# Kernel tuning notes

Measured on AMD Instinct MI355X. Metric: run time of the kernel, lower is better.

Reference implementation:

```python
import jax, jax.numpy as jnp
import numpy as np

B, N, IN_DIM, HID, OUT_DIM = 8, 1024, 768, 128, 768
H1, H2, MHA_HEADS, C = 8, 1, 4, 32
ALPHA = 0.2
NEG = -9e15
LN_EPS = 1e-5


def _gat_layer(x, W, a1, a2, adj_mask):
    # x: [B,N,Fin], W: [H,Fin,Fout], a1/a2: [H,Fout], adj_mask: [B,N,N] bool
    h = jnp.einsum('bni,hio->bhno', x, W)                      # [B,H,N,F]
    s1 = jnp.einsum('bhno,ho->bhn', h, a1)                     # score for source node i
    s2 = jnp.einsum('bhno,ho->bhn', h, a2)                     # score for target node j
    e = jax.nn.leaky_relu(s1[:, :, :, None] + s2[:, :, None, :], negative_slope=ALPHA)
    e = jnp.where(adj_mask[:, None, :, :], e, NEG)
    attn = jax.nn.softmax(e, axis=-1)                          # [B,H,N,N]
    hp = jnp.einsum('bhnm,bhmo->bhno', attn, h)                # [B,H,N,F]
    b, nh, n, f = hp.shape
    return hp.transpose(0, 2, 1, 3).reshape(b, n, nh * f)      # concat heads -> [B,N,H*F]


def _mha(q, k, v, wq, bq, wk, bk, wv, bv, wo, bo, n_heads):
    # torch-style MultiheadAttention (eval, no dropout). q:[B,Lq,E] k,v:[B,Lk,E]
    b, lq, e = q.shape
    lk = k.shape[1]
    hd = e // n_heads
    Q = (q @ wq + bq).reshape(b, lq, n_heads, hd).transpose(0, 2, 1, 3)
    K = (k @ wk + bk).reshape(b, lk, n_heads, hd).transpose(0, 2, 1, 3)
    V = (v @ wv + bv).reshape(b, lk, n_heads, hd).transpose(0, 2, 1, 3)
    scores = jnp.einsum('bhqd,bhkd->bhqk', Q, K) / jnp.sqrt(jnp.float32(hd))
    attn = jax.nn.softmax(scores, axis=-1)
    out = jnp.einsum('bhqk,bhkd->bhqd', attn, V)
    out = out.transpose(0, 2, 1, 3).reshape(b, lq, e)
    return out @ wo + bo


def _layernorm(x, g, b):
    mu = jnp.mean(x, axis=-1, keepdims=True)
    var = jnp.var(x, axis=-1, keepdims=True)
    return (x - mu) * jax.lax.rsqrt(var + LN_EPS) * g + b


def setup_inputs() -> dict:
    key = jax.random.key(0)
    ks = jax.random.split(key, 24)
    s = lambda fan_in: 1.0 / np.sqrt(fan_in)
    inp = {
        'node_features': jax.random.normal(ks[0], (B, N, IN_DIM), jnp.float32),
        'adjacency': jax.random.randint(ks[1], (B, N, N), 0, 2, jnp.int32),
        'context_indices': jax.random.randint(ks[2], (B, C), 0, N, jnp.int32),
        # GAT layer 1: 8 heads, in=768 -> out=128 each
        'W1': jax.random.normal(ks[3], (H1, IN_DIM, HID), jnp.float32) * s(IN_DIM),
        'a1_1': jax.random.normal(ks[4], (H1, HID), jnp.float32) * s(2 * HID),
        'a2_1': jax.random.normal(ks[5], (H1, HID), jnp.float32) * s(2 * HID),
        # GAT layer 2: 1 head, in=1024 -> out=128
        'W2': jax.random.normal(ks[6], (H2, HID * H1, HID), jnp.float32) * s(HID * H1),
        'a1_2': jax.random.normal(ks[7], (H2, HID), jnp.float32) * s(2 * HID),
        'a2_2': jax.random.normal(ks[8], (H2, HID), jnp.float32) * s(2 * HID),
        # query MultiheadAttention (embed_dim=128, 4 heads)
        'wq': jax.random.normal(ks[9], (HID, HID), jnp.float32) * s(HID),
        'bq': jnp.zeros((HID,), jnp.float32),
        'wk': jax.random.normal(ks[10], (HID, HID), jnp.float32) * s(HID),
        'bk': jnp.zeros((HID,), jnp.float32),
        'wv': jax.random.normal(ks[11], (HID, HID), jnp.float32) * s(HID),
        'bv': jnp.zeros((HID,), jnp.float32),
        'wo': jax.random.normal(ks[12], (HID, HID), jnp.float32) * s(HID),
        'bo': jnp.zeros((HID,), jnp.float32),
        # projection MLP
        'p1_w': jax.random.normal(ks[13], (HID, HID), jnp.float32) * s(HID),
        'p1_b': jnp.zeros((HID,), jnp.float32),
        'ln_g': jnp.ones((HID,), jnp.float32),
        'ln_b': jnp.zeros((HID,), jnp.float32),
        'p2_w': jax.random.normal(ks[14], (HID, OUT_DIM), jnp.float32) * s(HID),
        'p2_b': jnp.zeros((OUT_DIM,), jnp.float32),
    }
    return inp


def reference(node_features, adjacency, context_indices,
              W1, a1_1, a2_1, W2, a1_2, a2_2,
              wq, bq, wk, bk, wv, bv, wo, bo,
              p1_w, p1_b, ln_g, ln_b, p2_w, p2_b):
    adj_mask = adjacency > 0
    h = jax.nn.elu(_gat_layer(node_features, W1, a1_1, a2_1, adj_mask))  # [B,N,1024]
    h = jax.nn.elu(_gat_layer(h, W2, a1_2, a2_2, adj_mask))              # [B,N,128]
    q = h[:, 0:1, :]                                                      # [B,1,E]
    ctx = jnp.take_along_axis(h, context_indices[:, :, None], axis=1)     # [B,C,E]
    pooled = _mha(q, ctx, ctx, wq, bq, wk, bk, wv, bv, wo, bo, MHA_HEADS)[:, 0, :]
    z = jax.nn.relu(_layernorm(pooled @ p1_w + p1_b, ln_g, ln_b))
    return z @ p2_w + p2_b                                                # [B,OUT_DIM]
```

## Files before the change

### kernel.cpp

```cpp
#include <hip/hip_runtime.h>
#include <hip/hip_bf16.h>

#define ALPHA 0.2f
#define LOG2E 1.4426950408889634f

using short8  = __attribute__((ext_vector_type(8))) short;
using short4v = __attribute__((ext_vector_type(4))) short;
using f32x4   = __attribute__((ext_vector_type(4))) float;
using int4v   = __attribute__((ext_vector_type(4))) int;

static __device__ __forceinline__ float b2f(short s) {
    union { float f; unsigned u; } v; v.u = ((unsigned)(unsigned short)s) << 16; return v.f;
}
static __device__ __forceinline__ short f2bf(float f) {
    __hip_bfloat16 h = __float2bfloat16(f);
    return *reinterpret_cast<short*>(&h);
}
static __device__ __forceinline__ float fexp2(float x) {
    return __builtin_amdgcn_exp2f(x);
}
static __device__ __forceinline__ void gload_lds16(const void* g, void* l) {
    __builtin_amdgcn_global_load_lds(
        (const __attribute__((address_space(1))) unsigned*)g,
        (__attribute__((address_space(3))) unsigned*)l, 16, 0, 0);
}

__global__ __launch_bounds__(256) void k_prep(
        const int* __restrict__ adj, unsigned* __restrict__ adjb,
        const float* __restrict__ x, short* __restrict__ xb,
        const float* __restrict__ W1, short* __restrict__ W1T,
        const float* __restrict__ W2, short* __restrict__ W2T) {
    int bid = blockIdx.x, t = threadIdx.x;
    if (bid < 32768) {
        int idx = bid * 256 + t;
        int lane = t & 63;
        unsigned long long m = __ballot(adj[idx] > 0);
        if ((lane & 31) == 0) adjb[idx >> 5] = (unsigned)(m >> (lane & 32));
    } else if (bid < 38912) {
        int idx = (bid - 32768) * 256 + t;
        f32x4 v = ((const f32x4*)x)[idx];
        short4v o;
        o[0] = f2bf(v[0]); o[1] = f2bf(v[1]); o[2] = f2bf(v[2]); o[3] = f2bf(v[3]);
        ((short4v*)xb)[idx] = o;
    } else if (bid < 41984) {
        int idx = (bid - 38912) * 256 + t;
        int n = idx / 768, k = idx - n * 768;
        int h = n >> 7, o = n & 127;
        W1T[idx] = f2bf(W1[(h * 768 + k) * 128 + o]);
    } else {
        int idx = (bid - 41984) * 256 + t;
        int n = idx >> 10, k = idx & 1023;
        W2T[idx] = f2bf(W2[k * 128 + n]);
    }
}

__global__ __launch_bounds__(256) void k_gemm_bt(
        const short* __restrict__ A, const short* __restrict__ Bt,
        short* __restrict__ Ct, int K, int Ncols,
        const float* __restrict__ a1, const float* __restrict__ a2,
        float* __restrict__ s1, float* __restrict__ s2) {
    int tid = threadIdx.x, wave = tid >> 6, lane = tid & 63;
    int lr = lane & 15, lg = lane >> 4;
    int flat = blockIdx.y * gridDim.x + blockIdx.x;
    int chunkw = (gridDim.x * gridDim.y) >> 3;
    int swz = (flat & 7) * chunkw + (flat >> 3);
    int bx = swz % gridDim.x, by = swz / gridDim.x;
    int m0 = bx * 128, n0 = by * 128;
    int wm = (wave >> 1) * 64, wn = (wave & 1) * 64;
    __shared__ short lsA[2][128 * 64], lsB[2][128 * 64];
    __shared__ float sred1[2][128], sred2[2][128];
    f32x4 acc[4][4];
#pragma unroll
    for (int i = 0; i < 4; i++)
#pragma unroll
        for (int j = 0; j < 4; j++) acc[i][j] = (f32x4){0.f, 0.f, 0.f, 0.f};

    auto stage = [&](int bufsel, int k0) {
#pragma unroll
        for (int s = 0; s < 4; s++) {
            int chunk = s * 256 + tid;
            int r = chunk >> 3, c = chunk & 7;
            int csrc = c ^ (r & 7);
            gload_lds16(A + (size_t)(m0 + r) * K + k0 + csrc * 8, &lsA[bufsel][chunk * 8]);
            gload_lds16(Bt + (size_t)(n0 + r) * K + k0 + csrc * 8, &lsB[bufsel][chunk * 8]);
        }
    };
    auto compute = [&](const short* la, const short* lb) {
#pragma unroll
        for (int kk = 0; kk < 2; kk++) {
            short8 a[4], bb[4];
#pragma unroll
            for (int f = 0; f < 4; f++) {
                int ra = wm + f * 16 + lr, rb = wn + f * 16 + lr;
                a[f]  = *(const short8*)(la + ra * 64 + (((kk * 4 + lg) ^ (ra & 7)) * 8));
                bb[f] = *(const short8*)(lb + rb * 64 + (((kk * 4 + lg) ^ (rb & 7)) * 8));
            }
#pragma unroll
            for (int fm = 0; fm < 4; fm++)
#pragma unroll
                for (int fn = 0; fn < 4; fn++)
                    acc[fm][fn] = __builtin_amdgcn_mfma_f32_16x16x32_bf16(a[fm], bb[fn], acc[fm][fn], 0, 0, 0);
        }
    };
    stage(0, 0);
    __syncthreads();
    for (int k2 = 0; k2 < K; k2 += 128) {
        stage(1, k2 + 64);
        compute(lsA[0], lsB[0]);
        __syncthreads();
        if (k2 + 128 < K) stage(0, k2 + 128);
        compute(lsA[1], lsB[1]);
        __syncthreads();
    }
#pragma unroll
    for (int fm = 0; fm < 4; fm++) {
        int mb = m0 + wm + fm * 16 + lg * 4;
        size_t obase = ((size_t)(mb >> 10) * Ncols) * 1024 + (mb & 1023);
#pragma unroll
        for (int fn = 0; fn < 4; fn++) {
            int n = n0 + wn + fn * 16 + lr;
            short4v st;
            st[0] = f2bf(acc[fm][fn][0]); st[1] = f2bf(acc[fm][fn][1]);
            st[2] = f2bf(acc[fm][fn][2]); st[3] = f2bf(acc[fm][fn][3]);
            *(short4v*)(Ct + obase + (size_t)n * 1024) = st;
        }
    }
    if (a1 != nullptr) {
        int h = by;
        float av1[4], av2[4];
#pragma unroll
        for (int fn = 0; fn < 4; fn++) {
            int o = wn + fn * 16 + lr;
            av1[fn] = a1[h * 128 + o];
            av2[fn] = a2[h * 128 + o];
        }
        int wcol = wave & 1;
#pragma unroll
        for (int fm = 0; fm < 4; fm++)
#pragma unroll
            for (int r = 0; r < 4; r++) {
                float v1 = acc[fm][0][r] * av1[0] + acc[fm][1][r] * av1[1]
                         + acc[fm][2][r] * av1[2] + acc[fm][3][r] * av1[3];
                float v2 = acc[fm][0][r] * av2[0] + acc[fm][1][r] * av2[1]
                         + acc[fm][2][r] * av2[2] + acc[fm][3][r] * av2[3];
#pragma unroll
                for (int off = 1; off < 16; off <<= 1) {
                    v1 += __shfl_xor(v1, off);
                    v2 += __shfl_xor(v2, off);
                }
                if (lr == 0) {
                    int il = wm + fm * 16 + lg * 4 + r;
                    sred1[wcol][il] = v1;
                    sred2[wcol][il] = v2;
                }
            }
        __syncthreads();
        if (tid < 128) {
            int b = m0 >> 10;
            int irow = (b * 8 + h) * 1024 + (m0 & 1023) + tid;
            s1[irow] = (sred1[0][tid] + sred1[1][tid]) * LOG2E;
            s2[irow] = (sred2[0][tid] + sred2[1][tid]) * LOG2E;
        }
    }
}

__global__ __launch_bounds__(256) void k_gemm64(
        const short* __restrict__ A, const short* __restrict__ Bt,
        short* __restrict__ Ct, int K, int Ncols) {
    int tid = threadIdx.x, wave = tid >> 6, lane = tid & 63;
    int lr = lane & 15, lg = lane >> 4;
    int flat = blockIdx.y * gridDim.x + blockIdx.x;
    int chunkw = (gridDim.x * gridDim.y) >> 3;
    int swz = (flat & 7) * chunkw + (flat >> 3);
    int bx = swz % gridDim.x, by = swz / gridDim.x;
    int m0 = bx * 64, n0 = by * 64;
    int wm = (wave >> 1) * 32, wn = (wave & 1) * 32;
    __shared__ short lsA[2][64 * 32], lsB[2][64 * 32];
    f32x4 acc[2][2];
#pragma unroll
    for (int i = 0; i < 2; i++)
#pragma unroll
        for (int j = 0; j < 2; j++) acc[i][j] = (f32x4){0.f, 0.f, 0.f, 0.f};

    auto stage = [&](int bufsel, int k0) {
        int r = tid >> 2, c = tid & 3;
        int csrc = c ^ (r & 3);
        int base = (wave * 64) * 8;
        gload_lds16(A + (size_t)(m0 + r) * K + k0 + csrc * 8, &lsA[bufsel][base]);
        gload_lds16(Bt + (size_t)(n0 + r) * K + k0 + csrc * 8, &lsB[bufsel][base]);
    };
    stage(0, 0);
    __syncthreads();
    int buf = 0;
    for (int k0 = 0; k0 < K; k0 += 32) {
        if (k0 + 32 < K) stage(buf ^ 1, k0 + 32);
        short8 a[2], bb[2];
#pragma unroll
        for (int f = 0; f < 2; f++) {
            int ra = wm + f * 16 + lr, rb = wn + f * 16 + lr;
            a[f]  = *(const short8*)(&lsA[buf][ra * 32 + ((lg ^ (ra & 3)) * 8)]);
            bb[f] = *(const short8*)(&lsB[buf][rb * 32 + ((lg ^ (rb & 3)) * 8)]);
        }
#pragma unroll
        for (int fm = 0; fm < 2; fm++)
#pragma unroll
            for (int fn = 0; fn < 2; fn++)
                acc[fm][fn] = __builtin_amdgcn_mfma_f32_16x16x32_bf16(a[fm], bb[fn], acc[fm][fn], 0, 0, 0);
        __syncthreads();
        buf ^= 1;
    }
#pragma unroll
    for (int fm = 0; fm < 2; fm++) {
        int mb = m0 + wm + fm * 16 + lg * 4;
        size_t obase = ((size_t)(mb >> 10) * Ncols) * 1024 + (mb & 1023);
#pragma unroll
        for (int fn = 0; fn < 2; fn++) {
            int n = n0 + wn + fn * 16 + lr;
            short4v st;
            st[0] = f2bf(acc[fm][fn][0]); st[1] = f2bf(acc[fm][fn][1]);
            st[2] = f2bf(acc[fm][fn][2]); st[3] = f2bf(acc[fm][fn][3]);
            *(short4v*)(Ct + obase + (size_t)n * 1024) = st;
        }
    }
}

__global__ __launch_bounds__(256) void k_s12(
        const short* __restrict__ ht, const float* __restrict__ a1,
        const float* __restrict__ a2, float* __restrict__ s1,
        float* __restrict__ s2, int nh) {
    int bh = blockIdx.x;
    int h = bh % nh;
    int i4 = threadIdx.x * 4;
    const short* base = ht + (size_t)bh * 131072 + i4;
    f32x4 acc1 = {0.f, 0.f, 0.f, 0.f}, acc2 = {0.f, 0.f, 0.f, 0.f};
#pragma unroll 8
    for (int o = 0; o < 128; o++) {
        short4v v = *(const short4v*)(base + ((size_t)o << 10));
        float w1 = a1[h * 128 + o], w2 = a2[h * 128 + o];
#pragma unroll
        for (int r = 0; r < 4; r++) {
            float f = b2f(v[r]);
            acc1[r] += f * w1;
            acc2[r] += f * w2;
        }
    }
#pragma unroll
    for (int r = 0; r < 4; r++) { acc1[r] *= LOG2E; acc2[r] *= LOG2E; }
    *(f32x4*)(s1 + bh * 1024 + i4) = acc1;
    *(f32x4*)(s2 + bh * 1024 + i4) = acc2;
}

__global__ __launch_bounds__(512) void k_attn1(
        const short* __restrict__ ht, const unsigned* __restrict__ adjb,
        const float* __restrict__ s1, const float* __restrict__ s2,
        short* __restrict__ out) {
    int flat = blockIdx.y * 8 + blockIdx.x;
    int swz = (flat & 7) * 64 + (flat >> 3);
    int bh = swz >> 3, bxi = swz & 7;
    int b = bh >> 3, h = bh & 7;
    int tid = threadIdx.x, wave = tid >> 6, lane = tid & 63;
    int lr = lane & 15, lg = lane >> 4;
    int ic = bxi * 128 + wave * 16 + lr;
    int row = bh * 1024 + ic;
    float s1i = s1[row];
    const unsigned long long* abrow =
        (const unsigned long long*)(adjb + ((size_t)(b << 10) + ic) * 32);
    const float* s2r = s2 + bh * 1024;
    const short* hbase = ht + (size_t)bh * 131072;

    __shared__ short lsh[2][16384];
    f32x4 acc[8];
#pragma unroll
    for (int f = 0; f < 8; f++) acc[f] = (f32x4){0.f, 0.f, 0.f, 0.f};
    f32x4 accs = (f32x4){0.f, 0.f, 0.f, 0.f};
    short8 ones8;
#pragma unroll
    for (int e = 0; e < 8; e++) ones8[e] = (short)0x3F80;

    auto stage = [&](int bufsel, int j0) {
#pragma unroll
        for (int s = 0; s < 4; s++) {
            int chunk = s * 512 + tid;
            int r = chunk >> 4, c = chunk & 15;
            int csrc = c ^ (r & 15);
            gload_lds16(hbase + (size_t)r * 1024 + j0 + csrc * 8,
                        &lsh[bufsel][chunk * 8]);
        }
    };
    auto compute = [&](const short* ls, int j0) {
        unsigned long long aw0 = abrow[j0 >> 6], aw1 = abrow[(j0 >> 6) + 1];
#pragma unroll
        for (int kk = 0; kk < 4; kk++) {
            int jb = j0 + kk * 32 + lg * 8;
            f32x4 t0 = *(const f32x4*)(s2r + jb);
            f32x4 t1 = *(const f32x4*)(s2r + jb + 4);
            unsigned long long aw = (kk < 2) ? aw0 : aw1;
            unsigned bits = (unsigned)(aw >> ((kk & 1) * 32 + lg * 8)) & 0xFFu;
            float pv[8];
#pragma unroll
            for (int e = 0; e < 8; e++) {
                float sv = e < 4 ? t0[e] : t1[e & 3];
                float ee = s1i + sv;
                ee = fmaxf(ee, ALPHA * ee);
                float p = fexp2(ee);
                pv[e] = ((bits >> e) & 1) ? p : 0.f;
            }
            int4v pw;
#pragma unroll
            for (int w = 0; w < 4; w++) {
                int d;
                asm("v_cvt_pk_bf16_f32 %0, %1, %2"
                    : "=v"(d) : "v"(pv[2 * w]), "v"(pv[2 * w + 1]));
                pw[w] = d;
            }
            short8 pb = __builtin_bit_cast(short8, pw);
            accs = __builtin_amdgcn_mfma_f32_16x16x32_bf16(ones8, pb, accs, 0, 0, 0);
#pragma unroll
            for (int fm = 0; fm < 8; fm++) {
                int r = fm * 16 + lr;
                int ck = (kk * 4 + lg) ^ (r & 15);
                short8 af = *(const short8*)(ls + r * 128 + ck * 8);
                acc[fm] = __builtin_amdgcn_mfma_f32_16x16x32_bf16(af, pb, acc[fm], 0, 0, 0);
            }
        }
    };

    stage(0, 0);
    __syncthreads();
    for (int t2 = 0; t2 < 1024; t2 += 256) {
        stage(1, t2 + 128);
        compute(lsh[0], t2);
        __syncthreads();
        if (t2 + 256 < 1024) stage(0, t2 + 256);
        compute(lsh[1], t2 + 128);
        __syncthreads();
    }
    float rdi = 1.f / accs[0];
    size_t orow = ((size_t)(b << 10) + ic) * 1024 + h * 128;
#pragma unroll
    for (int fm = 0; fm < 8; fm++) {
        int ob = (fm << 4) + lg * 4;
        short4v st;
#pragma unroll
        for (int r = 0; r < 4; r++) {
            float x = acc[fm][r] * rdi;
            x = x > 0.f ? x : expm1f(x);
            st[r] = f2bf(x);
        }
        *(short4v*)(out + orow + ob) = st;
    }
}

__global__ __launch_bounds__(256) void k_attn2g(
        const short* __restrict__ h2t, const unsigned* __restrict__ adjb,
        const float* __restrict__ s1, const float* __restrict__ s2,
        const int* __restrict__ cidx, float* __restrict__ ghat) {
    int tile = blockIdx.x;
    int b = blockIdx.y;
    int tid = threadIdx.x, wave = tid >> 6, lane = tid & 63;
    int lr = lane & 15, lg = lane >> 4;

    __shared__ int nodes[16];
    __shared__ float sps[4][16];
    __shared__ float sacc[4][16][129];

    if (tid < 16) {
        int pos = tile * 16 + tid;
        int nd = 0;
        if (pos >= 1 && pos <= 32) nd = cidx[b * 32 + pos - 1];
        nodes[tid] = nd;
    }
    __syncthreads();

    const float* s2r = s2 + b * 1024;
    int nd = nodes[lr];
    float s1i = s1[b * 1024 + nd];
    const unsigned long long* abrow =
        (const unsigned long long*)(adjb + ((size_t)(b << 10) + nd) * 32);
    const short* hb = h2t + (size_t)b * 131072;
    f32x4 acc[8];
#pragma unroll
    for (int f = 0; f < 8; f++) acc[f] = (f32x4){0.f, 0.f, 0.f, 0.f};
    float psum = 0.f;

    for (int j0 = wave * 256; j0 < wave * 256 + 256; j0 += 32) {
        int jb = j0 + lg * 8;
        f32x4 t0 = *(const f32x4*)(s2r + jb);
        f32x4 t1 = *(const f32x4*)(s2r + jb + 4);
        unsigned bits = (unsigned)(abrow[j0 >> 6] >> ((j0 & 32) + lg * 8)) & 0xFFu;
        short8 pb;
#pragma unroll
        for (int e = 0; e < 8; e++) {
            float sv = e < 4 ? t0[e] : t1[e & 3];
            float ee = s1i + sv;
            ee = fmaxf(ee, ALPHA * ee);
            float p = fexp2(ee);
            p = ((bits >> e) & 1) ? p : 0.f;
            psum += p;
            pb[e] = f2bf(p);
        }
#pragma unroll
        for (int fm = 0; fm < 8; fm++) {
            short8 af = *(const short8*)(hb + (size_t)(fm * 16 + lr) * 1024 + jb);
            acc[fm] = __builtin_amdgcn_mfma_f32_16x16x32_bf16(af, pb, acc[fm], 0, 0, 0);
        }
    }
    psum += __shfl_xor(psum, 16);
    psum += __shfl_xor(psum, 32);
    if (lg == 0) sps[wave][lr] = psum;
#pragma unroll
    for (int fm = 0; fm < 8; fm++)
#pragma unroll
        for (int r = 0; r < 4; r++)
            sacc[wave][lr][fm * 16 + lg * 4 + r] = acc[fm][r];
    __syncthreads();
    for (int e = tid; e < 2048; e += 256) {
        int li = e >> 7, o = e & 127;
        float sum = sps[0][li] + sps[1][li] + sps[2][li] + sps[3][li];
        float v = (sacc[0][li][o] + sacc[1][li][o] + sacc[2][li][o] + sacc[3][li][o]) / sum;
        v = v > 0.f ? v : expm1f(v);
        ghat[((size_t)b * 48 + tile * 16 + li) * 128 + o] = v;
    }
}

__global__ __launch_bounds__(256) void k_qkv(
        const float* __restrict__ ghat,
        const float* __restrict__ wk, const float* __restrict__ bk,
        const float* __restrict__ wvp, const float* __restrict__ bv,
        float* __restrict__ Kp, float* __restrict__ Vp) {
    int b = blockIdx.y, rg = blockIdx.x & 7, o0 = (blockIdx.x >> 3) * 64;
    int t = threadIdx.x, wvi = t >> 6, ln = t & 63;
    __shared__ float sx[4][128];
    __shared__ float sWk[128 * 64], sWv[128 * 64];

    if (wvi < 2) {
        int cb = wvi * 64;
        gload_lds16(ghat + ((size_t)b * 48 + 1 + rg * 4) * 128 + (size_t)(cb + ln) * 4,
                    (float*)sx + cb * 4);
    }
#pragma unroll
    for (int s = 0; s < 8; s++) {
        int cb = s * 256 + wvi * 64;
        int q = cb + ln, rw = q >> 4, c4 = q & 15;
        gload_lds16(wk  + (size_t)rw * 128 + o0 + c4 * 4, &sWk[cb * 4]);
        gload_lds16(wvp + (size_t)rw * 128 + o0 + c4 * 4, &sWv[cb * 4]);
    }
    __syncthreads();
    int o = o0 + ln;
    float ka = bk[o], va = bv[o];
#pragma unroll 32
    for (int c = 0; c < 128; c++) {
        float x = sx[wvi][c];
        ka += x * sWk[c * 64 + ln];
        va += x * sWv[c * 64 + ln];
    }
    int r = rg * 4 + wvi;
    Kp[((size_t)b * 32 + r) * 128 + o] = ka;
    Vp[((size_t)b * 32 + r) * 128 + o] = va;
}

__global__ __launch_bounds__(256) void k_tail(
        const float* __restrict__ ghat, const float* __restrict__ Kp,
        const float* __restrict__ Vp,
        const float* __restrict__ wq, const float* __restrict__ bq,
        const float* __restrict__ wo, const float* __restrict__ bo,
        const float* __restrict__ p1w, const float* __restrict__ p1b,
        const float* __restrict__ lng, const float* __restrict__ lnb,
        float* __restrict__ tvec) {
    int b = blockIdx.x, t = threadIdx.x;
    int wvi = t >> 6, ln = t & 63;
    __shared__ float sq[128], sQ[128], sK[32][128], sV[32][128];
    __shared__ float sP[4][33], sO[128], sT[128], sZ[128];
    __shared__ float sred[2];
    __shared__ float sW[128 * 128];

#pragma unroll
    for (int s = 0; s < 4; s++) {
        int cb = s * 256 + wvi * 64;
        gload_lds16(Kp + (size_t)b * 4096 + (size_t)(cb + ln) * 4, (float*)sK + cb * 4);
        gload_lds16(Vp + (size_t)b * 4096 + (size_t)(cb + ln) * 4, (float*)sV + cb * 4);
    }
#pragma unroll
    for (int s = 0; s < 16; s++) {
        int cb = s * 256 + wvi * 64;
        gload_lds16(wq + (size_t)(cb + ln) * 4, &sW[cb * 4]);
    }
    if (t < 128) sq[t] = ghat[(size_t)b * 48 * 128 + t];
    __syncthreads();
    if (t < 128) {
        float a0 = 0.f, a1 = 0.f, a2 = 0.f, a3 = 0.f;
#pragma unroll
        for (int c = 0; c < 128; c += 4) {
            a0 += sq[c]     * sW[c * 128 + t];
            a1 += sq[c + 1] * sW[(c + 1) * 128 + t];
            a2 += sq[c + 2] * sW[(c + 2) * 128 + t];
            a3 += sq[c + 3] * sW[(c + 3) * 128 + t];
        }
        sQ[t] = bq[t] + ((a0 + a1) + (a2 + a3));
    }
    __syncthreads();
#pragma unroll
    for (int s = 0; s < 16; s++) {
        int cb = s * 256 + wvi * 64;
        gload_lds16(wo + (size_t)(cb + ln) * 4, &sW[cb * 4]);
    }
    if (t < 128) {
        int hh = t >> 5, jj = t & 31;
        float s = 0.f;
#pragma unroll
        for (int d = 0; d < 32; d++) s += sQ[hh * 32 + d] * sK[jj][hh * 32 + d];
        s *= 0.17677669529663687f;
        float m = s;
#pragma unroll
        for (int off = 16; off > 0; off >>= 1) m = fmaxf(m, __shfl_xor(m, off, 32));
        float p = __expf(s - m);
        float sum = p;
#pragma unroll
        for (int off = 16; off > 0; off >>= 1) sum += __shfl_xor(sum, off, 32);
        sP[hh][jj] = p / sum;
    }
    __syncthreads();
    if (t < 128) {
        int hh = t >> 5;
        float s = 0.f;
#pragma unroll
        for (int jj = 0; jj < 32; jj++) s += sP[hh][jj] * sV[jj][t];
        sO[t] = s;
    }
    __syncthreads();
    if (t < 128) {
        float a0 = 0.f, a1 = 0.f, a2 = 0.f, a3 = 0.f;
#pragma unroll
        for (int c = 0; c < 128; c += 4) {
            a0 += sO[c]     * sW[c * 128 + t];
            a1 += sO[c + 1] * sW[(c + 1) * 128 + t];
            a2 += sO[c + 2] * sW[(c + 2) * 128 + t];
            a3 += sO[c + 3] * sW[(c + 3) * 128 + t];
        }
        sT[t] = bo[t] + ((a0 + a1) + (a2 + a3));
    }
    __syncthreads();
#pragma unroll
    for (int s = 0; s < 16; s++) {
        int cb = s * 256 + wvi * 64;
        gload_lds16(p1w + (size_t)(cb + ln) * 4, &sW[cb * 4]);
    }
    __syncthreads();
    if (t < 128) {
        float a0 = 0.f, a1 = 0.f, a2 = 0.f, a3 = 0.f;
#pragma unroll
        for (int c = 0; c < 128; c += 4) {
            a0 += sT[c]     * sW[c * 128 + t];
            a1 += sT[c + 1] * sW[(c + 1) * 128 + t];
            a2 += sT[c + 2] * sW[(c + 2) * 128 + t];
            a3 += sT[c + 3] * sW[(c + 3) * 128 + t];
        }
        sZ[t] = p1b[t] + ((a0 + a1) + (a2 + a3));
    }
    __syncthreads();
    if (t < 64) {
        float v = sZ[t] + sZ[t + 64];
#pragma unroll
        for (int off = 32; off > 0; off >>= 1) v += __shfl_xor(v, off);
        if (t == 0) sred[0] = v * (1.f / 128.f);
    }
    __syncthreads();
    float mu = sred[0];
    if (t < 64) {
        float d1 = sZ[t] - mu, d2 = sZ[t + 64] - mu;
        float v = d1 * d1 + d2 * d2;
#pragma unroll
        for (int off = 32; off > 0; off >>= 1) v += __shfl_xor(v, off);
        if (t == 0) sred[1] = v * (1.f / 128.f);
    }
    __syncthreads();
    float rstd = rsqrtf(sred[1] + 1e-5f);
    if (t < 128) {
        float z = (sZ[t] - mu) * rstd * lng[t] + lnb[t];
        tvec[b * 128 + t] = fmaxf(z, 0.f);
    }
}

__global__ __launch_bounds__(256) void k_p2(
        const float* __restrict__ tvec, const float* __restrict__ p2w,
        const float* __restrict__ p2b, float* __restrict__ out) {
    int jj0 = blockIdx.x * 128, b = blockIdx.y;
    int t = threadIdx.x, wvi = t >> 6, ln = t & 63;
    __shared__ float sT[128];
    __shared__ float sW[128 * 128];

#pragma unroll
    for (int s = 0; s < 16; s++) {
        int cb = s * 256 + wvi * 64;
        int q = cb + ln, c = q >> 5, c4 = q & 31;
        gload_lds16(p2w + (size_t)c * 768 + jj0 + c4 * 4, &sW[cb * 4]);
    }
    if (t < 128) sT[t] = tvec[b * 128 + t];
    __syncthreads();
    if (t < 128) {
        float a0 = 0.f, a1 = 0.f, a2 = 0.f, a3 = 0.f;
#pragma unroll
        for (int c = 0; c < 128; c += 4) {
            a0 += sT[c]     * sW[c * 128 + t];
            a1 += sT[c + 1] * sW[(c + 1) * 128 + t];
            a2 += sT[c + 2] * sW[(c + 2) * 128 + t];
            a3 += sT[c + 3] * sW[(c + 3) * 128 + t];
        }
        out[b * 768 + jj0 + t] = p2b[jj0 + t] + ((a0 + a1) + (a2 + a3));
    }
}

extern "C" void kernel_launch(void* const* d_in, const int* in_sizes, int n_in,
                              void* d_out, int out_size, void* d_ws, size_t ws_size,
                              hipStream_t stream) {
    const float* x   = (const float*)d_in[0];
    const int*  adj  = (const int*)d_in[1];
    const int*  cidx = (const int*)d_in[2];
    const float* W1  = (const float*)d_in[3];
    const float* a11 = (const float*)d_in[4];
    const float* a21 = (const float*)d_in[5];
    const float* W2  = (const float*)d_in[6];
    const float* a12 = (const float*)d_in[7];
    const float* a22 = (const float*)d_in[8];
    const float* wq = (const float*)d_in[9];  const float* bq = (const float*)d_in[10];
    const float* wk = (const float*)d_in[11]; const float* bk = (const float*)d_in[12];
    const float* wv = (const float*)d_in[13]; const float* bv = (const float*)d_in[14];
    const float* wo = (const float*)d_in[15]; const float* bo = (const float*)d_in[16];
    const float* p1w = (const float*)d_in[17]; const float* p1b = (const float*)d_in[18];
    const float* lng = (const float*)d_in[19]; const float* lnb = (const float*)d_in[20];
    const float* p2w = (const float*)d_in[21]; const float* p2b = (const float*)d_in[22];
    float* out = (float*)d_out;

    char* ws = (char*)d_ws;
    size_t off = 0;
    auto alloc = [&](size_t bytes) -> char* {
        char* p = ws + off;
        off = (off + bytes + 255) & ~(size_t)255;
        return p;
    };
    short* Xb   = (short*)alloc(8192ull * 768 * 2);
    short* W1T  = (short*)alloc(1024ull * 768 * 2);
    short* W2T  = (short*)alloc(128ull * 1024 * 2);
    unsigned* adjb = (unsigned*)alloc(8ull * 1024 * 32 * 4);
    short* h1t  = (short*)alloc(64ull * 128 * 1024 * 2);
    float* s1a  = (float*)alloc(64ull * 1024 * 4);
    float* s2a  = (float*)alloc(64ull * 1024 * 4);
    short* hcat = (short*)alloc(8192ull * 1024 * 2);
    short* h2t  = (short*)alloc(8ull * 128 * 1024 * 2);
    float* s1b  = (float*)alloc(8192ull * 4);
    float* s2b  = (float*)alloc(8192ull * 4);
    float* ghat = (float*)alloc(8ull * 48 * 128 * 4);
    float* Kp   = (float*)alloc(8ull * 32 * 128 * 4);
    float* Vp   = (float*)alloc(8ull * 32 * 128 * 4);
    float* tvec = (float*)alloc(8ull * 128 * 4);
    if (off > ws_size) return;

    k_prep<<<42496, 256, 0, stream>>>(adj, adjb, x, Xb, W1, W1T, W2, W2T);

    k_gemm_bt<<<dim3(64, 8), 256, 0, stream>>>(Xb, W1T, h1t, 768, 1024,
                                               a11, a21, s1a, s2a);
    k_attn1<<<dim3(8, 64), 512, 0, stream>>>(h1t, adjb, s1a, s2a, hcat);

    k_gemm64<<<dim3(128, 2), 256, 0, stream>>>(hcat, W2T, h2t, 1024, 128);
    k_s12<<<8, 256, 0, stream>>>(h2t, a12, a22, s1b, s2b, 1);
    k_attn2g<<<dim3(3, 8), 256, 0, stream>>>(h2t, adjb, s1b, s2b, cidx, ghat);

    k_qkv<<<dim3(16, 8), 256, 0, stream>>>(ghat, wk, bk, wv, bv, Kp, Vp);
    k_tail<<<8, 256, 0, stream>>>(ghat, Kp, Vp, wq, bq, wo, bo,
                                  p1w, p1b, lng, lnb, tvec);
    k_p2<<<dim3(6, 8), 256, 0, stream>>>(tvec, p2w, p2b, out);
}
```

Before: 155.6 us.

## Stage GEMM epilogue through LDS for coalesced stores; cache s2 in LDS; add setprio

The projection GEMM epilogue now writes its bf16 tile into LDS with an XOR swizzle, then reads it back so each thread emits 16-byte contiguous global stores along the node dimension. This replaces the scattered 8-byte transposed stores. The attention kernel also preloads the per-head s2 score vector into shared memory once, so the inner loop no longer reads it from global memory. Its MFMA block is wrapped in s_setprio to favour matrix issue. The costs are an extra barrier and LDS traffic in the epilogue, plus 4KB more shared memory per block, which could reduce occupancy.

```diff
diff --git a/kernel.cpp b/kernel.cpp
--- a/kernel.cpp
+++ b/kernel.cpp
@@ -112,18 +112,32 @@
         compute(lsA[1], lsB[1]);
         __syncthreads();
     }
+    short* stg = &lsA[0][0];
 #pragma unroll
     for (int fm = 0; fm < 4; fm++) {
-        int mb = m0 + wm + fm * 16 + lg * 4;
-        size_t obase = ((size_t)(mb >> 10) * Ncols) * 1024 + (mb & 1023);
 #pragma unroll
         for (int fn = 0; fn < 4; fn++) {
-            int n = n0 + wn + fn * 16 + lr;
+            int nl = wn + fn * 16 + lr;
+            int i4w = (wm + fm * 16 + lg * 4) >> 2;
             short4v st;
             st[0] = f2bf(acc[fm][fn][0]); st[1] = f2bf(acc[fm][fn][1]);
             st[2] = f2bf(acc[fm][fn][2]); st[3] = f2bf(acc[fm][fn][3]);
-            *(short4v*)(Ct + obase + (size_t)n * 1024) = st;
-        }
+            *(short4v*)(stg + (nl * 32 + (i4w ^ (nl & 31))) * 4) = st;
+        }
+    }
+    __syncthreads();
+    size_t gbase = ((size_t)(m0 >> 10) * Ncols + n0) * 1024 + (m0 & 1023);
+#pragma unroll
+    for (int it = 0; it < 8; it++) {
+        int idx8 = it * 256 + tid;
+        int nl = idx8 >> 4, p = idx8 & 15;
+        int i4a = 2 * p, i4b = 2 * p + 1;
+        short4v lo = *(short4v*)(stg + (nl * 32 + (i4a ^ (nl & 31))) * 4);
+        short4v hi = *(short4v*)(stg + (nl * 32 + (i4b ^ (nl & 31))) * 4);
+        short8 v;
+#pragma unroll
+        for (int r = 0; r < 4; r++) { v[r] = lo[r]; v[r + 4] = hi[r]; }
+        *(short8*)(Ct + gbase + (size_t)nl * 1024 + p * 8) = v;
     }
     if (a1 != nullptr) {
         int h = by;
@@ -269,6 +283,7 @@
     const short* hbase = ht + (size_t)bh * 131072;
 
     __shared__ short lsh[2][16384];
+    __shared__ float ls2[1024];
     f32x4 acc[8];
 #pragma unroll
     for (int f = 0; f < 8; f++) acc[f] = (f32x4){0.f, 0.f, 0.f, 0.f};
@@ -292,8 +307,8 @@
 #pragma unroll
         for (int kk = 0; kk < 4; kk++) {
             int jb = j0 + kk * 32 + lg * 8;
-            f32x4 t0 = *(const f32x4*)(s2r + jb);
-            f32x4 t1 = *(const f32x4*)(s2r + jb + 4);
+            f32x4 t0 = *(const f32x4*)(&ls2[jb]);
+            f32x4 t1 = *(const f32x4*)(&ls2[jb + 4]);
             unsigned long long aw = (kk < 2) ? aw0 : aw1;
             unsigned bits = (unsigned)(aw >> ((kk & 1) * 32 + lg * 8)) & 0xFFu;
             float pv[8];
@@ -314,6 +329,7 @@
                 pw[w] = d;
             }
             short8 pb = __builtin_bit_cast(short8, pw);
+            __builtin_amdgcn_s_setprio(1);
             accs = __builtin_amdgcn_mfma_f32_16x16x32_bf16(ones8, pb, accs, 0, 0, 0);
 #pragma unroll
             for (int fm = 0; fm < 8; fm++) {
@@ -322,9 +338,13 @@
                 short8 af = *(const short8*)(ls + r * 128 + ck * 8);
                 acc[fm] = __builtin_amdgcn_mfma_f32_16x16x32_bf16(af, pb, acc[fm], 0, 0, 0);
             }
+            __builtin_amdgcn_s_setprio(0);
         }
     };
 
+    if (wave < 4) {
+        gload_lds16(s2r + (wave * 64 + lane) * 4, &ls2[wave * 256]);
+    }
     stage(0, 0);
     __syncthreads();
     for (int t2 = 0; t2 < 1024; t2 += 256) {
```

Result: faster. 148.1 us (-4.9%).
